# Performance work log

Hardware: AMD Instinct MI355X
Metric: run time of the kernel (lower is better)

The kernel has to match this reference:

```python
import jax, jax.numpy as jnp
import numpy as np

B, N, C, H = 4, 1024, 1024, 16
HD = C // H


def setup_inputs() -> dict:
    key = jax.random.key(0)
    ks = jax.random.split(key, 9)
    s = 0.02
    return {
        "x": jax.random.normal(ks[0], (B, N, C), dtype=jnp.float32),
        "qkv_w": jax.random.normal(ks[1], (3 * C, C), dtype=jnp.float32) * s,
        "qkv_b": jax.random.normal(ks[2], (3 * C,), dtype=jnp.float32) * s,
        "proj_w": jax.random.normal(ks[3], (C, C), dtype=jnp.float32) * s,
        "proj_b": jax.random.normal(ks[4], (C,), dtype=jnp.float32) * s,
        "wl": jax.random.normal(ks[5], (H, H), dtype=jnp.float32) * s,
        "bl": jax.random.normal(ks[6], (H,), dtype=jnp.float32) * s,
        "ww": jax.random.normal(ks[7], (H, H), dtype=jnp.float32) * s,
        "bw": jax.random.normal(ks[8], (H,), dtype=jnp.float32) * s,
    }


def reference(x, qkv_w, qkv_b, proj_w, proj_b, wl, bl, ww, bw):
    # qkv: torch Linear convention y = x @ W.T + b
    scale = HD ** (-0.5)
    qkv = (jnp.einsum("bnc,oc->bno", x, qkv_w) + qkv_b)
    qkv = qkv.reshape(B, N, 3, H, HD).transpose(2, 0, 3, 1, 4)  # [3,B,H,N,HD]
    q, k, v = qkv[0] * scale, qkv[1], qkv[2]
    attn = jnp.einsum("bhnd,bhmd->bhnm", q, k)  # [B,H,N,N]
    # talking-heads mix before softmax (proj_l over head dim)
    attn = jnp.einsum("bhnm,gh->bgnm", attn, wl) + bl[:, None, None]
    attn = jax.nn.softmax(attn, axis=-1)
    # talking-heads mix after softmax (proj_w over head dim)
    attn = jnp.einsum("bhnm,gh->bgnm", attn, ww) + bw[:, None, None]
    out = jnp.einsum("bhnm,bhmd->bhnd", attn, v)  # [B,H,N,HD]
    out = out.transpose(0, 2, 1, 3).reshape(B, N, C)
    out = jnp.einsum("bnc,oc->bno", out, proj_w) + proj_b
    return out, attn
```

## Files before the change

### kernel.cpp

```cpp
#include <hip/hip_runtime.h>
#include <hip/hip_bf16.h>

typedef unsigned short u16;
typedef __attribute__((ext_vector_type(8))) __bf16 bf16x8;
typedef __attribute__((ext_vector_type(4))) float f32x4;
typedef __attribute__((ext_vector_type(2))) float f32x2;

template <typename T> struct is16 { static constexpr bool v = false; };
template <> struct is16<u16> { static constexpr bool v = true; };

__device__ __forceinline__ float bf2f(u16 u) {
    unsigned int x = ((unsigned int)u) << 16;
    return __builtin_bit_cast(float, x);
}
__device__ __forceinline__ u16 f2bf(float f) {
    unsigned int x = __builtin_bit_cast(unsigned int, f);
    unsigned int lsb = (x >> 16) & 1u;
    x += 0x7fffu + lsb;
    return (u16)(x >> 16);
}
__device__ __forceinline__ float bf2f_lo(unsigned int u) { return __builtin_bit_cast(float, u << 16); }
__device__ __forceinline__ float bf2f_hi(unsigned int u) { return __builtin_bit_cast(float, u & 0xffff0000u); }

__device__ __forceinline__ void ld8(u16* dst, const u16* src) {
    *(float4*)dst = *(const float4*)src;
}
__device__ __forceinline__ void ld8(u16* dst, const float* src) {
    float4 a = *(const float4*)src;
    float4 b = *(const float4*)(src + 4);
    u16 t[8];
    t[0] = f2bf(a.x); t[1] = f2bf(a.y); t[2] = f2bf(a.z); t[3] = f2bf(a.w);
    t[4] = f2bf(b.x); t[5] = f2bf(b.y); t[6] = f2bf(b.z); t[7] = f2bf(b.w);
    *(float4*)dst = *(float4*)t;
}
__device__ __forceinline__ void stC(u16* p, float v)   { *p = f2bf(v); }
__device__ __forceinline__ void stC(float* p, float v) { *p = v; }

__device__ __forceinline__ void g2l16(const void* g, void* l) {
    __builtin_amdgcn_global_load_lds(
        (const __attribute__((address_space(1))) void*)g,
        (__attribute__((address_space(3))) void*)l, 16, 0, 0);
}

__global__ __launch_bounds__(256)
void cvt_all(const float* __restrict__ x, const float* __restrict__ qw,
             const float* __restrict__ pw, u16* __restrict__ xb,
             u16* __restrict__ qwb, u16* __restrict__ pwb)
{
    long long t = (long long)blockIdx.x * 256 + threadIdx.x;
    const float* src; u16* dst; long long o;
    if (t < 524288)      { src = x;  dst = xb;  o = t; }
    else if (t < 917504) { src = qw; dst = qwb; o = t - 524288; }
    else                 { src = pw; dst = pwb; o = t - 917504; }
    u16 tmp[8];
    ld8(tmp, src + o * 8);
    *(float4*)(dst + o * 8) = *(float4*)tmp;
}

template <typename TA, typename TB, typename TC, int BN = 128>
__global__ __launch_bounds__(256)
void gemm_nt(const TA* __restrict__ A, long long sAb, long long sAh, int lda,
             const TB* __restrict__ B, long long sBb, long long sBh, int ldb,
             TC* __restrict__ C, long long sCb, long long sCh, int ldc,
             const float* __restrict__ bias, int K, int zdiv,
             float cscale, int csplit)
{
    constexpr int SA = is16<TA>::v ? 32 : 40;
    constexpr int SB = is16<TB>::v ? 32 : 40;
    constexpr int MI = (BN == 128) ? 4 : 2;
    __shared__ u16 As[128 * SA];
    __shared__ u16 Bs[BN * SB];

    const int tid = threadIdx.x;
    const int z = blockIdx.z;
    const int zb = z / zdiv, zh = z % zdiv;
    A += zb * sAb + zh * sAh;
    B += zb * sBb + zh * sBh;
    C += zb * sCb + zh * sCh;
    const int m0 = blockIdx.y * 128;
    const int n0 = blockIdx.x * BN;
    const int wid = tid >> 6;
    const int lane = tid & 63;
    const int wm = (BN == 128) ? (wid >> 1) * 64 : wid * 32;
    const int wn = (BN == 128) ? (wid & 1) * 64 : 0;
    const int lr = lane & 15;
    const int quad = lane >> 4;

    f32x4 acc[MI][4];
#pragma unroll
    for (int i = 0; i < MI; i++)
#pragma unroll
        for (int j = 0; j < 4; j++)
#pragma unroll
            for (int r = 0; r < 4; r++) acc[i][j][r] = 0.f;

    const int srow = tid >> 2;
    const int scol = (tid & 3) * 8;

    for (int k0 = 0; k0 < K; k0 += 32) {
        __syncthreads();
        const TA* ga = A + (long long)(m0 + srow) * lda + k0 + scol;
        if constexpr (is16<TA>::v) {
            g2l16(ga, (char*)As + tid * 16);
            g2l16(ga + (long long)64 * lda, (char*)As + 4096 + tid * 16);
        } else {
            ld8(&As[srow * SA + scol], ga);
            ld8(&As[(srow + 64) * SA + scol], ga + (long long)64 * lda);
        }
        const TB* gb = B + (long long)(n0 + srow) * ldb + k0 + scol;
        if constexpr (is16<TB>::v) {
            g2l16(gb, (char*)Bs + tid * 16);
            if constexpr (BN == 128)
                g2l16(gb + (long long)64 * ldb, (char*)Bs + 4096 + tid * 16);
        } else {
            ld8(&Bs[srow * SB + scol], gb);
            if constexpr (BN == 128)
                ld8(&Bs[(srow + 64) * SB + scol], gb + (long long)64 * ldb);
        }
        __syncthreads();

        bf16x8 af[MI], bfr[4];
#pragma unroll
        for (int t = 0; t < MI; t++)
            af[t]  = *(const bf16x8*)&As[(wm + t * 16 + lr) * SA + quad * 8];
#pragma unroll
        for (int t = 0; t < 4; t++)
            bfr[t] = *(const bf16x8*)&Bs[(wn + t * 16 + lr) * SB + quad * 8];
#pragma unroll
        for (int i = 0; i < MI; i++)
#pragma unroll
            for (int j = 0; j < 4; j++)
                acc[i][j] = __builtin_amdgcn_mfma_f32_16x16x32_bf16(af[i], bfr[j], acc[i][j], 0, 0, 0);
    }

#pragma unroll
    for (int j = 0; j < 4; j++) {
        const int col = n0 + wn + j * 16 + lr;
        const float bv = bias ? bias[col] : 0.f;
        const float scl = (col < csplit) ? cscale : 1.f;
#pragma unroll
        for (int i = 0; i < MI; i++) {
            const int rbase = m0 + wm + i * 16 + quad * 4;
#pragma unroll
            for (int r = 0; r < 4; r++)
                stC(&C[(long long)(rbase + r) * ldc + col], (acc[i][j][r] + bv) * scl);
        }
    }
}

__global__ __launch_bounds__(256)
void qk_gemm(const u16* __restrict__ q, const u16* __restrict__ k,
             u16* __restrict__ s)
{
    __shared__ u16 As[2 * 128 * 32];
    __shared__ u16 Bs[2 * 128 * 32];

    const int tid = threadIdx.x;
    const int z = blockIdx.z;
    const int zb = z >> 4, zh = z & 15;
    const u16* Q = q + (long long)zb * 3145728 + zh * 64;
    const u16* Kv = k + (long long)zb * 3145728 + zh * 64;
    u16* C = s + (long long)z * 1048576;
    const int m0 = blockIdx.y * 128;
    const int n0 = blockIdx.x * 128;
    const int wid = tid >> 6;
    const int lane = tid & 63;
    const int wm = (wid >> 1) * 64;
    const int wn = (wid & 1) * 64;
    const int lr = lane & 15;
    const int quad = lane >> 4;
    const int srow = tid >> 2;
    const int scol = (tid & 3) * 8;

#pragma unroll
    for (int c = 0; c < 2; c++) {
        const u16* ga = Q + (long long)(m0 + srow) * 3072 + c * 32 + scol;
        g2l16(ga, (char*)As + c * 8192 + tid * 16);
        g2l16(ga + (long long)64 * 3072, (char*)As + c * 8192 + 4096 + tid * 16);
        const u16* gb = Kv + (long long)(n0 + srow) * 3072 + c * 32 + scol;
        g2l16(gb, (char*)Bs + c * 8192 + tid * 16);
        g2l16(gb + (long long)64 * 3072, (char*)Bs + c * 8192 + 4096 + tid * 16);
    }
    __syncthreads();

    f32x4 acc[4][4];
#pragma unroll
    for (int i = 0; i < 4; i++)
#pragma unroll
        for (int j = 0; j < 4; j++)
#pragma unroll
            for (int r = 0; r < 4; r++) acc[i][j][r] = 0.f;

#pragma unroll
    for (int c = 0; c < 2; c++) {
        bf16x8 af[4], bfr[4];
#pragma unroll
        for (int t = 0; t < 4; t++) {
            af[t]  = *(const bf16x8*)&As[c * 4096 + (wm + t * 16 + lr) * 32 + quad * 8];
            bfr[t] = *(const bf16x8*)&Bs[c * 4096 + (wn + t * 16 + lr) * 32 + quad * 8];
        }
#pragma unroll
        for (int i = 0; i < 4; i++)
#pragma unroll
            for (int j = 0; j < 4; j++)
                acc[i][j] = __builtin_amdgcn_mfma_f32_16x16x32_bf16(af[i], bfr[j], acc[i][j], 0, 0, 0);
    }

#pragma unroll
    for (int j = 0; j < 4; j++) {
        const int col = n0 + wn + j * 16 + lr;
#pragma unroll
        for (int i = 0; i < 4; i++) {
            const int rbase = m0 + wm + i * 16 + quad * 4;
#pragma unroll
            for (int r = 0; r < 4; r++)
                C[(long long)(rbase + r) * 1024 + col] = f2bf(acc[i][j][r]);
        }
    }
}

__global__ __launch_bounds__(256)
void mix_softmax(const u16* __restrict__ S, float* __restrict__ attn_out,
                 u16* __restrict__ attn_bf,
                 const float* __restrict__ wl, const float* __restrict__ bl,
                 const float* __restrict__ ww, const float* __restrict__ bw)
{
    __shared__ u16 Ss[16 * 1024];
    __shared__ float wlT[256];
    __shared__ float wwT[256];
    __shared__ float blS[16];
    __shared__ float bwS[16];
    __shared__ float red[64];
    __shared__ float gsum[16];

    const int tid = threadIdx.x;
    const int lane = tid & 63;
    const int wid = tid >> 6;
    const int b = blockIdx.x >> 10, n = blockIdx.x & 1023;

    const long long base0 = ((long long)(b * 16) * 1024 + n) * 1024;

#pragma unroll
    for (int j = 0; j < 8; j++) {
        const int h = j * 2 + (tid >> 7);
        const int c8 = tid & 127;
        g2l16(S + base0 + (long long)h * 1048576 + c8 * 8,
              (char*)Ss + j * 4096 + tid * 16);
    }

    wlT[(tid & 15) * 16 + (tid >> 4)] = wl[tid];
    if (tid < 16) { blS[tid] = bl[tid]; bwS[tid] = bw[tid]; }
    __syncthreads();

    float lsum[16];
#pragma unroll
    for (int g = 0; g < 16; g++) lsum[g] = 0.f;

#pragma unroll
    for (int ph = 0; ph < 2; ph++) {
        const int c0 = ph * 512 + tid * 2;
        f32x2 a[16];
#pragma unroll
        for (int g = 0; g < 16; g++) {
            float bv = blS[g];
            a[g] = (f32x2){bv, bv};
        }
#pragma unroll
        for (int h = 0; h < 16; h++) {
            unsigned int r = *(const unsigned int*)&Ss[h * 1024 + c0];
            f32x2 sv;
            sv.x = bf2f_lo(r);
            sv.y = bf2f_hi(r);
            float wr[16];
            *(f32x4*)&wr[0]  = *(const f32x4*)&wlT[h * 16];
            *(f32x4*)&wr[4]  = *(const f32x4*)&wlT[h * 16 + 4];
            *(f32x4*)&wr[8]  = *(const f32x4*)&wlT[h * 16 + 8];
            *(f32x4*)&wr[12] = *(const f32x4*)&wlT[h * 16 + 12];
#pragma unroll
            for (int g = 0; g < 16; g++)
                a[g] += sv * wr[g];
        }
#pragma unroll
        for (int g = 0; g < 16; g++) {
            float px = __expf(a[g].x);
            float py = __expf(a[g].y);
            lsum[g] += px + py;
            unsigned int bo = ((unsigned int)f2bf(py) << 16) | (unsigned int)f2bf(px);
            *(unsigned int*)&Ss[g * 1024 + c0] = bo;
        }
    }

#pragma unroll
    for (int g = 0; g < 16; g++) {
        float vv = lsum[g];
        for (int off = 32; off; off >>= 1) vv += __shfl_xor(vv, off, 64);
        if (lane == 0) red[wid * 16 + g] = vv;
    }
    __syncthreads();
    if (tid < 16)
        gsum[tid] = (red[tid] + red[16 + tid]) + (red[32 + tid] + red[48 + tid]);
    __syncthreads();
    wwT[(tid & 15) * 16 + (tid >> 4)] = ww[tid] / gsum[tid & 15];
    __syncthreads();

#pragma unroll
    for (int ph = 0; ph < 2; ph++) {
        const int c0 = ph * 512 + tid * 2;
        f32x2 o[16];
#pragma unroll
        for (int g = 0; g < 16; g++) {
            float bv = bwS[g];
            o[g] = (f32x2){bv, bv};
        }
#pragma unroll
        for (int h = 0; h < 16; h++) {
            unsigned int r = *(const unsigned int*)&Ss[h * 1024 + c0];
            f32x2 e;
            e.x = bf2f_lo(r);
            e.y = bf2f_hi(r);
            float wr[16];
            *(f32x4*)&wr[0]  = *(const f32x4*)&wwT[h * 16];
            *(f32x4*)&wr[4]  = *(const f32x4*)&wwT[h * 16 + 4];
            *(f32x4*)&wr[8]  = *(const f32x4*)&wwT[h * 16 + 8];
            *(f32x4*)&wr[12] = *(const f32x4*)&wwT[h * 16 + 12];
#pragma unroll
            for (int g = 0; g < 16; g++)
                o[g] += e * wr[g];
        }
#pragma unroll
        for (int g = 0; g < 16; g++) {
            const long long off = base0 + c0 + (long long)g * 1048576;
            __builtin_nontemporal_store(o[g], (f32x2*)(attn_out + off));
            unsigned int bo = ((unsigned int)f2bf(o[g].y) << 16) | (unsigned int)f2bf(o[g].x);
            *(unsigned int*)(attn_bf + off) = bo;
        }
    }
}

__global__ __launch_bounds__(256)
void av_gemm(const u16* __restrict__ attn_bf, const u16* __restrict__ y,
             u16* __restrict__ out1)
{
    __shared__ u16 As[64 * 32];
    __shared__ u16 Bs[64 * 40];

    const int tid = threadIdx.x;
    const int z = blockIdx.z;
    const int b = z >> 4, h = z & 15;
    const int m0 = blockIdx.x * 64;
    const u16* Ab = attn_bf + (long long)z * 1048576;
    const u16* Vb = y + (long long)b * 3145728 + 2048 + h * 64;
    const int wid = tid >> 6;
    const int lane = tid & 63;
    const int lr = lane & 15;
    const int quad = lane >> 4;
    const int wm = wid * 16;

    f32x4 acc[4];
#pragma unroll
    for (int j = 0; j < 4; j++)
#pragma unroll
        for (int r = 0; r < 4; r++) acc[j][r] = 0.f;

    const int srow = tid >> 2;
    const int scol = (tid & 3) * 8;
    const int vrow = tid >> 3;
    const int vdb = (tid & 7) * 8;

    for (int k0 = 0; k0 < 1024; k0 += 32) {
        __syncthreads();
        g2l16(Ab + (long long)(m0 + srow) * 1024 + k0 + scol, (char*)As + tid * 16);
        u16 tmp[8];
        *(float4*)tmp = *(const float4*)(Vb + (long long)(k0 + vrow) * 3072 + vdb);
#pragma unroll
        for (int j = 0; j < 8; j++) Bs[(vdb + j) * 40 + vrow] = tmp[j];
        __syncthreads();

        bf16x8 af, bfr[4];
        af = *(const bf16x8*)&As[(wm + lr) * 32 + quad * 8];
#pragma unroll
        for (int t = 0; t < 4; t++)
            bfr[t] = *(const bf16x8*)&Bs[(t * 16 + lr) * 40 + quad * 8];
#pragma unroll
        for (int j = 0; j < 4; j++)
            acc[j] = __builtin_amdgcn_mfma_f32_16x16x32_bf16(af, bfr[j], acc[j], 0, 0, 0);
    }

#pragma unroll
    for (int j = 0; j < 4; j++) {
        const int col = h * 64 + j * 16 + lr;
        const int rbase = m0 + wm + quad * 4;
#pragma unroll
        for (int r = 0; r < 4; r++)
            out1[(long long)(b * 1024 + rbase + r) * 1024 + col] = f2bf(acc[j][r]);
    }
}

extern "C" void kernel_launch(void* const* d_in, const int* in_sizes, int n_in,
                              void* d_out, int out_size, void* d_ws, size_t ws_size,
                              hipStream_t stream)
{
    const float* x      = (const float*)d_in[0];
    const float* qkv_w  = (const float*)d_in[1];
    const float* qkv_b  = (const float*)d_in[2];
    const float* proj_w = (const float*)d_in[3];
    const float* proj_b = (const float*)d_in[4];
    const float* wl     = (const float*)d_in[5];
    const float* bl     = (const float*)d_in[6];
    const float* ww     = (const float*)d_in[7];
    const float* bw     = (const float*)d_in[8];

    float* out      = (float*)d_out;
    float* attn_out = out + 4194304;

    u16* ws   = (u16*)d_ws;
    u16* y    = ws;
    u16* out1 = ws + 12582912;
    u16* pwb  = ws + 16777216;
    u16* s    = ws + 25165824;
    u16* xb   = s;
    u16* qwb  = s + 4194304;

    dim3 blk(256);
    cvt_all<<<dim3(4096), blk, 0, stream>>>(x, qkv_w, proj_w, xb, qwb, pwb);
    gemm_nt<u16, u16, u16, 128><<<dim3(24, 32, 1), blk, 0, stream>>>(
        xb, 0, 0, 1024, qwb, 0, 0, 1024, y, 0, 0, 3072, qkv_b, 1024, 1, 0.125f, 1024);
    qk_gemm<<<dim3(8, 8, 64), blk, 0, stream>>>(y, y + 1024, s);
    mix_softmax<<<dim3(4096), blk, 0, stream>>>(s, attn_out, s, wl, bl, ww, bw);
    av_gemm<<<dim3(16, 1, 64), blk, 0, stream>>>(s, y, out1);
    gemm_nt<u16, u16, float, 64><<<dim3(16, 32, 1), blk, 0, stream>>>(
        out1, 0, 0, 1024, pwb, 0, 0, 1024, out, 0, 0, 1024, proj_b, 1024, 1, 1.f, 0);
}
```

Before: 529.1 us.

## Enlarge av_gemm M tile to 128 rows and prefetch V into registers

```diff
diff --git a/kernel.cpp b/kernel.cpp
--- a/kernel.cpp
+++ b/kernel.cpp
@@ -341,58 +341,73 @@
 void av_gemm(const u16* __restrict__ attn_bf, const u16* __restrict__ y,
              u16* __restrict__ out1)
 {
-    __shared__ u16 As[64 * 32];
+    __shared__ u16 As[128 * 32];
     __shared__ u16 Bs[64 * 40];
 
     const int tid = threadIdx.x;
     const int z = blockIdx.z;
     const int b = z >> 4, h = z & 15;
-    const int m0 = blockIdx.x * 64;
+    const int m0 = blockIdx.x * 128;
     const u16* Ab = attn_bf + (long long)z * 1048576;
     const u16* Vb = y + (long long)b * 3145728 + 2048 + h * 64;
     const int wid = tid >> 6;
     const int lane = tid & 63;
     const int lr = lane & 15;
     const int quad = lane >> 4;
-    const int wm = wid * 16;
-
-    f32x4 acc[4];
-#pragma unroll
-    for (int j = 0; j < 4; j++)
-#pragma unroll
-        for (int r = 0; r < 4; r++) acc[j][r] = 0.f;
+    const int wm = wid * 32;
+
+    f32x4 acc[2][4];
+#pragma unroll
+    for (int i = 0; i < 2; i++)
+#pragma unroll
+        for (int j = 0; j < 4; j++)
+#pragma unroll
+            for (int r = 0; r < 4; r++) acc[i][j][r] = 0.f;
 
     const int srow = tid >> 2;
     const int scol = (tid & 3) * 8;
     const int vrow = tid >> 3;
     const int vdb = (tid & 7) * 8;
 
+    u16 vtmp[8];
+    *(float4*)vtmp = *(const float4*)(Vb + (long long)vrow * 3072 + vdb);
+
     for (int k0 = 0; k0 < 1024; k0 += 32) {
         __syncthreads();
-        g2l16(Ab + (long long)(m0 + srow) * 1024 + k0 + scol, (char*)As + tid * 16);
-        u16 tmp[8];
-        *(float4*)tmp = *(const float4*)(Vb + (long long)(k0 + vrow) * 3072 + vdb);
-#pragma unroll
-        for (int j = 0; j < 8; j++) Bs[(vdb + j) * 40 + vrow] = tmp[j];
+        g2l16(Ab + (long long)(m0 + srow) * 1024 + k0 + scol,
+              (char*)As + tid * 16);
+        g2l16(Ab + (long long)(m0 + 64 + srow) * 1024 + k0 + scol,
+              (char*)As + 4096 + tid * 16);
+#pragma unroll
+        for (int j = 0; j < 8; j++) Bs[(vdb + j) * 40 + vrow] = vtmp[j];
         __syncthreads();
 
-        bf16x8 af, bfr[4];
-        af = *(const bf16x8*)&As[(wm + lr) * 32 + quad * 8];
+        if (k0 + 32 < 1024)
+            *(float4*)vtmp = *(const float4*)(Vb + (long long)(k0 + 32 + vrow) * 3072 + vdb);
+
+        bf16x8 af[2], bfr[4];
+        af[0] = *(const bf16x8*)&As[(wm + lr) * 32 + quad * 8];
+        af[1] = *(const bf16x8*)&As[(wm + 16 + lr) * 32 + quad * 8];
 #pragma unroll
         for (int t = 0; t < 4; t++)
             bfr[t] = *(const bf16x8*)&Bs[(t * 16 + lr) * 40 + quad * 8];
 #pragma unroll
-        for (int j = 0; j < 4; j++)
-            acc[j] = __builtin_amdgcn_mfma_f32_16x16x32_bf16(af, bfr[j], acc[j], 0, 0, 0);
+        for (int i = 0; i < 2; i++)
+#pragma unroll
+            for (int j = 0; j < 4; j++)
+                acc[i][j] = __builtin_amdgcn_mfma_f32_16x16x32_bf16(af[i], bfr[j], acc[i][j], 0, 0, 0);
     }
 
 #pragma unroll
     for (int j = 0; j < 4; j++) {
         const int col = h * 64 + j * 16 + lr;
-        const int rbase = m0 + wm + quad * 4;
-#pragma unroll
-        for (int r = 0; r < 4; r++)
-            out1[(long long)(b * 1024 + rbase + r) * 1024 + col] = f2bf(acc[j][r]);
+#pragma unroll
+        for (int i = 0; i < 2; i++) {
+            const int rbase = m0 + wm + i * 16 + quad * 4;
+#pragma unroll
+            for (int r = 0; r < 4; r++)
+                out1[(long long)(b * 1024 + rbase + r) * 1024 + col] = f2bf(acc[i][j][r]);
+        }
     }
 }
 
@@ -427,7 +442,7 @@
         xb, 0, 0, 1024, qwb, 0, 0, 1024, y, 0, 0, 3072, qkv_b, 1024, 1, 0.125f, 1024);
     qk_gemm<<<dim3(8, 8, 64), blk, 0, stream>>>(y, y + 1024, s);
     mix_softmax<<<dim3(4096), blk, 0, stream>>>(s, attn_out, s, wl, bl, ww, bw);
-    av_gemm<<<dim3(16, 1, 64), blk, 0, stream>>>(s, y, out1);
+    av_gemm<<<dim3(8, 1, 64), blk, 0, stream>>>(s, y, out1);
     gemm_nt<u16, u16, float, 64><<<dim3(16, 32, 1), blk, 0, stream>>>(
         out1, 0, 0, 1024, pwb, 0, 0, 1024, out, 0, 0, 1024, proj_b, 1024, 1, 1.f, 0);
 }
```

Result: faster. 514.8 us (-2.7%).
